# Kernel tuning notes

Hardware: AMD Instinct MI355X
Metric: run time of the kernel (lower is better)

## Reference

```python
import jax, jax.numpy as jnp
import numpy as np

N_HEAD = 16
EPS = 1e-6


def setup_inputs() -> dict:
    key = jax.random.key(0)
    k1, k2, k3 = jax.random.split(key, 3)
    B, T, C = 2, 2048, 1024
    x = jax.random.normal(k1, (B, T, C), dtype=jnp.float32)
    w_attn = jax.random.normal(k2, (C, 3 * C), dtype=jnp.float32) * 0.02
    w_proj = jax.random.normal(k3, (C, C), dtype=jnp.float32) * 0.02
    return {"x": x, "w_attn": w_attn, "w_proj": w_proj}


def _linear_attention(q, k, v):
    """q,k,v: (T,B,H,D) with q,k already feature-mapped (elu+1).
    Causal linear attention via a D x D running-state recurrence (same math
    as cumsum of k-v outer products, computed without the O(T*D^2) tensor)."""
    B, H, D = q.shape[1], q.shape[2], q.shape[3]

    def step(carry, qkv_t):
        S, z = carry                      # S:(B,H,D,D), z:(B,H,D)
        qt, kt, vt = qkv_t                # each (B,H,D)
        S = S + kt[..., :, None] * vt[..., None, :]
        z = z + kt
        num = jnp.einsum('bhi,bhij->bhj', qt, S)
        den = jnp.sum(qt * z, axis=-1, keepdims=True)
        return (S, z), num / (den + EPS)

    S0 = jnp.zeros((B, H, D, D), q.dtype)
    z0 = jnp.zeros((B, H, D), q.dtype)
    _, y = jax.lax.scan(step, (S0, z0), (q, k, v))
    return y                              # (T,B,H,D)


def reference(x, w_attn, w_proj):
    B, T, C = x.shape
    H = N_HEAD
    D = C // H
    qkv = x @ w_attn                      # (B,T,3C)
    q, k, v = jnp.split(qkv, 3, axis=-1)

    def to_tbhd(a):                       # (B,T,C) -> (T,B,H,D)
        return a.reshape(B, T, H, D).transpose(1, 0, 2, 3)

    q = jax.nn.elu(to_tbhd(q)) + 1.0      # phi(x) = ELU(x)+1
    k = jax.nn.elu(to_tbhd(k)) + 1.0
    v = to_tbhd(v)

    y = _linear_attention(q, k, v)        # (T,B,H,D)
    y = y.transpose(1, 0, 2, 3).reshape(B, T, C)
    return y @ w_proj                     # resid dropout p=0.0 is identity
```

## Files before the change

kernel.cpp:

```cpp
#include <hip/hip_runtime.h>
#include <hip/hip_bf16.h>
#include <cmath>

#define TB   2048
#define CCH  1024
#define NCH  32
#define EPSF 1e-6f

typedef unsigned short u16;
typedef __attribute__((ext_vector_type(8))) short  frag8;
typedef __attribute__((ext_vector_type(4))) float  floatx4;

__device__ __forceinline__ u16 f2bf(float f) {
    unsigned int u = __float_as_uint(f);
    unsigned int r = (u + 0x7fffu + ((u >> 16) & 1u)) >> 16;
    return (u16)r;
}
__device__ __forceinline__ float bf2f(u16 v) {
    return __uint_as_float(((unsigned int)v) << 16);
}

__device__ __forceinline__ void async_load16(const u16* g, u16* l) {
    __builtin_amdgcn_global_load_lds(
        (const __attribute__((address_space(1))) void*)g,
        (__attribute__((address_space(3))) void*)l,
        16, 0, 0);
}

__global__ __launch_bounds__(256) void prep_k(
    const float* __restrict__ x, const float* __restrict__ wa,
    const float* __restrict__ wp,
    u16* __restrict__ xb, u16* __restrict__ waT, u16* __restrict__ wpT)
{
    __shared__ u16 t[64][72];
    int blk = blockIdx.x;
    if (blk < 2048) {
        int i = (blk * 256 + threadIdx.x) * 8;
        float4 a = *(const float4*)(x + i);
        float4 b = *(const float4*)(x + i + 4);
        u16 v[8];
        v[0] = f2bf(a.x); v[1] = f2bf(a.y); v[2] = f2bf(a.z); v[3] = f2bf(a.w);
        v[4] = f2bf(b.x); v[5] = f2bf(b.y); v[6] = f2bf(b.z); v[7] = f2bf(b.w);
        *(uint4*)(xb + i) = *(uint4*)v;
        return;
    }
    const float* in; u16* out; int K, N, bx, by;
    if (blk < 2048 + 768) {
        int tb = blk - 2048; in = wa; out = waT; K = 1024; N = 3072;
        bx = tb % 48; by = tb / 48;
    } else {
        int tb = blk - 2816; in = wp; out = wpT; K = 1024; N = 1024;
        bx = tb & 15; by = tb >> 4;
    }
    const int k0 = by * 64, n0 = bx * 64;
    #pragma unroll
    for (int i = 0; i < 4; ++i) {
        int rr = (threadIdx.x >> 4) + 16 * i;
        int c4 = (threadIdx.x & 15) * 4;
        float4 v = *(const float4*)(in + (size_t)(k0 + rr) * N + n0 + c4);
        t[c4 + 0][rr] = f2bf(v.x);
        t[c4 + 1][rr] = f2bf(v.y);
        t[c4 + 2][rr] = f2bf(v.z);
        t[c4 + 3][rr] = f2bf(v.w);
    }
    __syncthreads();
    #pragma unroll
    for (int i = 0; i < 2; ++i) {
        int rr = (threadIdx.x >> 3) + 32 * i;
        int c8 = (threadIdx.x & 7) * 8;
        u16 o[8];
        #pragma unroll
        for (int q = 0; q < 8; ++q) o[q] = t[rr][c8 + q];
        *(uint4*)(out + (size_t)(n0 + rr) * K + k0 + c8) = *(uint4*)o;
    }
}

__global__ __launch_bounds__(256) void gemm_bf16_bf16out_k(
    const u16* __restrict__ A, const u16* __restrict__ BT,
    u16* __restrict__ C, int N, int K, int phi_cols)
{
    __shared__ u16 Als[128 * 64];
    __shared__ u16 Bls[128 * 64];
    const int tid  = threadIdx.x;
    const int wave = tid >> 6, lane = tid & 63;
    const int quad = lane >> 4, lrow = lane & 15;
    const int wm = wave >> 1, wn = wave & 1;
    const int row0 = blockIdx.y * 128, col0 = blockIdx.x * 128;
    const int lr = lane >> 3;
    const int lc = ((lane & 7) ^ lr) * 8;
    const int rsw = lrow & 7;
    floatx4 acc[4][4] = {};

    for (int k0 = 0; k0 < K; k0 += 64) {
        __syncthreads();
        #pragma unroll
        for (int m = 0; m < 4; ++m) {
            int i = wave * 4 + m;
            async_load16(A  + (size_t)(row0 + i * 8 + lr) * K + k0 + lc, &Als[i * 512]);
            async_load16(BT + (size_t)(col0 + i * 8 + lr) * K + k0 + lc, &Bls[i * 512]);
        }
        __syncthreads();
        #pragma unroll
        for (int ksi = 0; ksi < 2; ++ksi) {
            frag8 af[4], bf[4];
            #pragma unroll
            for (int i = 0; i < 4; ++i)
                af[i] = *(const frag8*)&Als[(wm * 64 + i * 16 + lrow) * 64
                                            + ((ksi * 4 + quad) ^ rsw) * 8];
            #pragma unroll
            for (int i = 0; i < 4; ++i)
                bf[i] = *(const frag8*)&Bls[(wn * 64 + i * 16 + lrow) * 64
                                            + ((ksi * 4 + quad) ^ rsw) * 8];
            #pragma unroll
            for (int i = 0; i < 4; ++i)
                #pragma unroll
                for (int jn = 0; jn < 4; ++jn)
                    acc[i][jn] = __builtin_amdgcn_mfma_f32_16x16x32_bf16(
                        af[i], bf[jn], acc[i][jn], 0, 0, 0);
        }
    }

    #pragma unroll
    for (int i = 0; i < 4; ++i) {
        #pragma unroll
        for (int jn = 0; jn < 4; ++jn) {
            int col = col0 + wn * 64 + jn * 16 + lrow;
            bool isphi = col < phi_cols;
            #pragma unroll
            for (int r = 0; r < 4; ++r) {
                int row = row0 + wm * 64 + i * 16 + quad * 4 + r;
                float v = acc[i][jn][r];
                if (isphi) v = (v > 0.f) ? (v + 1.f) : __expf(v);
                C[(size_t)row * N + col] = f2bf(v);
            }
        }
    }
}

__global__ __launch_bounds__(256) void gemm_bf16_f32out_k(
    const u16* __restrict__ A, const u16* __restrict__ BT,
    float* __restrict__ C, int N, int K)
{
    __shared__ u16 Als[128 * 128];
    __shared__ u16 Bls[64 * 128];
    const int tid  = threadIdx.x;
    const int wave = tid >> 6, lane = tid & 63;
    const int quad = lane >> 4, lrow = lane & 15;
    const int wm = wave >> 1, wn = wave & 1;
    const int row0 = blockIdx.y * 128, col0 = blockIdx.x * 64;
    const int lr4 = lane >> 4;
    floatx4 acc[4][2] = {};

    for (int k0 = 0; k0 < K; k0 += 128) {
        __syncthreads();
        #pragma unroll
        for (int m = 0; m < 8; ++m) {
            int rbase = wave * 32 + m * 4;
            int cg = (lane & 15) ^ ((rbase + lr4) & 15);
            async_load16(A + (size_t)(row0 + rbase + lr4) * K + k0 + cg * 8,
                         &Als[rbase * 128]);
        }
        #pragma unroll
        for (int m = 0; m < 4; ++m) {
            int rbase = wave * 16 + m * 4;
            int cg = (lane & 15) ^ ((rbase + lr4) & 15);
            async_load16(BT + (size_t)(col0 + rbase + lr4) * K + k0 + cg * 8,
                         &Bls[rbase * 128]);
        }
        __syncthreads();
        #pragma unroll
        for (int ksi = 0; ksi < 4; ++ksi) {
            frag8 af[4], bf[2];
            #pragma unroll
            for (int i = 0; i < 4; ++i)
                af[i] = *(const frag8*)&Als[(wm * 64 + i * 16 + lrow) * 128
                                            + ((ksi * 4 + quad) ^ lrow) * 8];
            #pragma unroll
            for (int jn = 0; jn < 2; ++jn)
                bf[jn] = *(const frag8*)&Bls[(wn * 32 + jn * 16 + lrow) * 128
                                             + ((ksi * 4 + quad) ^ lrow) * 8];
            #pragma unroll
            for (int i = 0; i < 4; ++i)
                #pragma unroll
                for (int jn = 0; jn < 2; ++jn)
                    acc[i][jn] = __builtin_amdgcn_mfma_f32_16x16x32_bf16(
                        af[i], bf[jn], acc[i][jn], 0, 0, 0);
        }
    }

    #pragma unroll
    for (int i = 0; i < 4; ++i)
        #pragma unroll
        for (int jn = 0; jn < 2; ++jn) {
            int col = col0 + wn * 32 + jn * 16 + lrow;
            #pragma unroll
            for (int r = 0; r < 4; ++r) {
                int row = row0 + wm * 64 + i * 16 + quad * 4 + r;
                C[(size_t)row * N + col] = acc[i][jn][r];
            }
        }
}

__global__ __launch_bounds__(256) void chunk_kv_mfma_k(
    const u16* __restrict__ qkv,
    u16* __restrict__ Spt,
    float* __restrict__ zloc,
    u16* __restrict__ VtG)
{
    __shared__ u16 Kt[64][72];
    __shared__ u16 Vt[64][72];
    const int tid  = threadIdx.x;
    const int wave = tid >> 6, lane = tid & 63;
    const int quad = lane >> 4, lrow = lane & 15;
    const int blk = blockIdx.x;
    const int c = blk & 31, h = (blk >> 5) & 15, b = blk >> 9;
    const int t0 = c * 64;
    const u16* base = qkv + (size_t)(b * TB + t0) * 3072 + h * 64;

    #pragma unroll
    for (int m = 0; m < 2; ++m) {
        int chunk = tid + 256 * m;
        int s = chunk >> 3, d0 = (chunk & 7) * 8;
        const u16* row = base + (size_t)s * 3072;
        u16 kv[8], vv[8];
        *(uint4*)kv = *(const uint4*)(row + 1024 + d0);
        *(uint4*)vv = *(const uint4*)(row + 2048 + d0);
        #pragma unroll
        for (int q = 0; q < 8; ++q) { Kt[d0 + q][s] = kv[q]; Vt[d0 + q][s] = vv[q]; }
    }
    __syncthreads();

    #pragma unroll
    for (int m = 0; m < 2; ++m) {
        int e = tid + 256 * m;
        int r = e >> 3, c8 = (e & 7) * 8;
        u16 o[8];
        #pragma unroll
        for (int q = 0; q < 8; ++q) o[q] = Vt[r][c8 + q];
        *(uint4*)(VtG + (size_t)blk * 4096 + r * 64 + c8) = *(uint4*)o;
    }

    frag8 vf[2];
    #pragma unroll
    for (int ks = 0; ks < 2; ++ks)
        vf[ks] = *(const frag8*)&Vt[wave * 16 + lrow][ks * 32 + quad * 8];
    u16* So = Spt + (size_t)blk * 4096;
    #pragma unroll
    for (int jn = 0; jn < 4; ++jn) {
        floatx4 acc = {};
        #pragma unroll
        for (int ks = 0; ks < 2; ++ks) {
            frag8 kf = *(const frag8*)&Kt[jn * 16 + lrow][ks * 32 + quad * 8];
            acc = __builtin_amdgcn_mfma_f32_16x16x32_bf16(vf[ks], kf, acc, 0, 0, 0);
        }
        #pragma unroll
        for (int r = 0; r < 4; ++r) {
            int j = wave * 16 + quad * 4 + r;
            int i = jn * 16 + lrow;
            So[j * 64 + i] = f2bf(acc[r]);
        }
    }
    if (tid < 64) {
        float z = 0.f;
        for (int s = 0; s < 64; ++s) z += bf2f(Kt[tid][s]);
        zloc[(size_t)blk * 64 + tid] = z;
    }
}

__global__ __launch_bounds__(256) void scan_state_k(
    u16* __restrict__ Spt, float* __restrict__ z)
{
    const int bh = blockIdx.x >> 1;
    const int part = blockIdx.x & 1;
    const int e0 = part * 2048 + threadIdx.x * 8;
    const size_t base = (size_t)bh * NCH * 4096;
    float r[8] = {};
    for (int c = 0; c < NCH; ++c) {
        u16* p = Spt + base + (size_t)c * 4096 + e0;
        u16 t[8];
        *(uint4*)t = *(const uint4*)p;
        u16 o[8];
        #pragma unroll
        for (int q = 0; q < 8; ++q) { o[q] = f2bf(r[q]); r[q] += bf2f(t[q]); }
        *(uint4*)p = *(uint4*)o;
    }
    if (part == 0 && threadIdx.x < 64) {
        const size_t zb = (size_t)bh * NCH * 64;
        float rz = 0.f;
        for (int c = 0; c < NCH; ++c) {
            float t = z[zb + c * 64 + threadIdx.x];
            z[zb + c * 64 + threadIdx.x] = rz;
            rz += t;
        }
    }
}

__global__ __launch_bounds__(256) void attn_mfma_k(
    const u16* __restrict__ qkv,
    const u16* __restrict__ SptG,
    const float* __restrict__ zp,
    const u16* __restrict__ VtG,
    u16* __restrict__ Yb)
{
    __shared__ u16 Qls[64 * 64];
    __shared__ u16 Kls[64 * 64];
    __shared__ u16 Vls[64 * 64];
    __shared__ u16 Sls[64 * 64];
    __shared__ float zps[64];
    __shared__ float den4[64][4];
    __shared__ float den[64];

    const int tid  = threadIdx.x;
    const int wave = tid >> 6, lane = tid & 63;
    const int quad = lane >> 4, lrow = lane & 15;
    const int blk = blockIdx.x;
    const int c = blk & 31, h = (blk >> 5) & 15, b = blk >> 9;
    const int t0 = c * 64;
    const int lr = lane >> 3;
    const int lc = ((lane & 7) ^ lr) * 8;
    const int rsw = lrow & 7;
    const u16* qbase = qkv + (size_t)(b * TB + t0) * 3072 + h * 64;

    #pragma unroll
    for (int m = 0; m < 2; ++m) {
        int i = wave * 2 + m;
        int r = i * 8 + lr;
        async_load16(qbase + (size_t)r * 3072 + lc,          &Qls[i * 512]);
        async_load16(qbase + (size_t)r * 3072 + 1024 + lc,   &Kls[i * 512]);
        async_load16(SptG + (size_t)blk * 4096 + r * 64 + lc, &Sls[i * 512]);
        async_load16(VtG  + (size_t)blk * 4096 + r * 64 + lc, &Vls[i * 512]);
    }
    if (tid < 64) zps[tid] = zp[(size_t)blk * 64 + tid];
    __syncthreads();

    frag8 qf[2];
    #pragma unroll
    for (int ks = 0; ks < 2; ++ks)
        qf[ks] = *(const frag8*)&Qls[(wave * 16 + lrow) * 64 + ((ks * 4 + quad) ^ rsw) * 8];

    floatx4 yacc[4] = {}, kacc[4] = {};
    #pragma unroll
    for (int jn = 0; jn < 4; ++jn) {
        #pragma unroll
        for (int ks = 0; ks < 2; ++ks) {
            frag8 spf = *(const frag8*)&Sls[(jn * 16 + lrow) * 64 + ((ks * 4 + quad) ^ rsw) * 8];
            yacc[jn] = __builtin_amdgcn_mfma_f32_16x16x32_bf16(qf[ks], spf, yacc[jn], 0, 0, 0);
            frag8 kf = *(const frag8*)&Kls[(jn * 16 + lrow) * 64 + ((ks * 4 + quad) ^ rsw) * 8];
            kacc[jn] = __builtin_amdgcn_mfma_f32_16x16x32_bf16(qf[ks], kf, kacc[jn], 0, 0, 0);
        }
    }
    __syncthreads();

    #pragma unroll
    for (int jn = 0; jn < 4; ++jn) {
        int s = jn * 16 + lrow;
        #pragma unroll
        for (int r = 0; r < 4; ++r) {
            int t = wave * 16 + quad * 4 + r;
            float v = (s <= t) ? kacc[jn][r] : 0.f;
            Sls[t * 64 + (((s >> 3) ^ (t & 7)) * 8) + (s & 7)] = f2bf(v);
        }
    }
    __syncthreads();

    {
        int t = tid >> 2, seg = tid & 3;
        float p = 0.f;
        #pragma unroll
        for (int g2 = 0; g2 < 2; ++g2) {
            int g = seg * 2 + g2;
            int pq = ((g ^ (t & 7)) * 8);
            const u16* qp = &Qls[t * 64 + pq];
            const u16* ap = &Sls[t * 64 + pq];
            #pragma unroll
            for (int e = 0; e < 8; ++e) {
                p += bf2f(qp[e]) * zps[g * 8 + e] + bf2f(ap[e]);
            }
        }
        den4[t][seg] = p;
    }

    frag8 af2[2];
    #pragma unroll
    for (int ks = 0; ks < 2; ++ks)
        af2[ks] = *(const frag8*)&Sls[(wave * 16 + lrow) * 64 + ((ks * 4 + quad) ^ rsw) * 8];
    #pragma unroll
    for (int jn = 0; jn < 4; ++jn)
        #pragma unroll
        for (int ks = 0; ks < 2; ++ks) {
            frag8 vf = *(const frag8*)&Vls[(jn * 16 + lrow) * 64 + ((ks * 4 + quad) ^ rsw) * 8];
            yacc[jn] = __builtin_amdgcn_mfma_f32_16x16x32_bf16(af2[ks], vf, yacc[jn], 0, 0, 0);
        }
    __syncthreads();
    if (tid < 64) den[tid] = den4[tid][0] + den4[tid][1] + den4[tid][2] + den4[tid][3];
    __syncthreads();

    #pragma unroll
    for (int jn = 0; jn < 4; ++jn) {
        #pragma unroll
        for (int r = 0; r < 4; ++r) {
            int t = wave * 16 + quad * 4 + r;
            float inv = 1.f / (den[t] + EPSF);
            Qls[t * 64 + jn * 16 + lrow] = f2bf(yacc[jn][r] * inv);
        }
    }
    __syncthreads();
    {
        int row = tid >> 2, seg = tid & 3;
        size_t o = (size_t)(b * TB + t0 + row) * CCH + h * 64 + seg * 16;
        *(uint4*)(Yb + o)     = *(uint4*)&Qls[row * 64 + seg * 16];
        *(uint4*)(Yb + o + 8) = *(uint4*)&Qls[row * 64 + seg * 16 + 8];
    }
}

extern "C" void kernel_launch(void* const* d_in, const int* in_sizes, int n_in,
                              void* d_out, int out_size, void* d_ws, size_t ws_size,
                              hipStream_t stream)
{
    const float* x      = (const float*)d_in[0];
    const float* w_attn = (const float*)d_in[1];
    const float* w_proj = (const float*)d_in[2];
    float* out = (float*)d_out;

    u16* xb    = (u16*)d_ws;
    u16* waT   = xb    + (size_t)4096 * 1024;
    u16* wpT   = waT   + (size_t)3072 * 1024;
    u16* Yb    = wpT   + (size_t)1024 * 1024;
    u16* qkv_b = Yb    + (size_t)4096 * 1024;
    u16* Spt   = qkv_b + (size_t)4096 * 3072;
    u16* VtG   = Spt   + (size_t)1024 * 4096;
    float* zloc = (float*)(VtG + (size_t)1024 * 4096);

    prep_k<<<3072, 256, 0, stream>>>(x, w_attn, w_proj, xb, waT, wpT);

    gemm_bf16_bf16out_k<<<dim3(24, 32), 256, 0, stream>>>(xb, waT, qkv_b, 3072, 1024, 2048);

    chunk_kv_mfma_k<<<1024, 256, 0, stream>>>(qkv_b, Spt, zloc, VtG);
    scan_state_k   <<<64,   256, 0, stream>>>(Spt, zloc);
    attn_mfma_k    <<<1024, 256, 0, stream>>>(qkv_b, Spt, zloc, VtG, Yb);

    gemm_bf16_f32out_k<<<dim3(16, 32), 256, 0, stream>>>(Yb, wpT, out, 1024, 1024);
}
```

Baseline: 169.6 us.

## Double-buffer LDS tiles in bf16 GEMM to overlap global loads with MFMA

Converts the QKV/projection GEMM main loop to double-buffered shared memory. The next K-tile is fetched with async global-to-LDS loads while the current tile is consumed, using explicit vmcnt waits and barriers. This is meant to hide global load latency behind MFMA work. It doubles LDS use to 64KB per block, which may reduce occupancy, and it relies on hand-counted waitcnt values being correct.

```diff
diff --git a/kernel.cpp b/kernel.cpp
--- a/kernel.cpp
+++ b/kernel.cpp
@@ -79,8 +79,8 @@
     const u16* __restrict__ A, const u16* __restrict__ BT,
     u16* __restrict__ C, int N, int K, int phi_cols)
 {
-    __shared__ u16 Als[128 * 64];
-    __shared__ u16 Bls[128 * 64];
+    __shared__ u16 Als[2][128 * 64];
+    __shared__ u16 Bls[2][128 * 64];
     const int tid  = threadIdx.x;
     const int wave = tid >> 6, lane = tid & 63;
     const int quad = lane >> 4, lrow = lane & 15;
@@ -90,27 +90,46 @@
     const int lc = ((lane & 7) ^ lr) * 8;
     const int rsw = lrow & 7;
     floatx4 acc[4][4] = {};
-
-    for (int k0 = 0; k0 < K; k0 += 64) {
-        __syncthreads();
-        #pragma unroll
-        for (int m = 0; m < 4; ++m) {
-            int i = wave * 4 + m;
-            async_load16(A  + (size_t)(row0 + i * 8 + lr) * K + k0 + lc, &Als[i * 512]);
-            async_load16(BT + (size_t)(col0 + i * 8 + lr) * K + k0 + lc, &Bls[i * 512]);
-        }
-        __syncthreads();
+    const int NT = K >> 6;
+
+    #pragma unroll
+    for (int m = 0; m < 4; ++m) {
+        int i = wave * 4 + m;
+        async_load16(A  + (size_t)(row0 + i * 8 + lr) * K + lc, &Als[0][i * 512]);
+        async_load16(BT + (size_t)(col0 + i * 8 + lr) * K + lc, &Bls[0][i * 512]);
+    }
+
+    for (int t = 0; t < NT; ++t) {
+        const int p = t & 1;
+        if (t + 1 < NT) {
+            const int k0 = (t + 1) << 6;
+            #pragma unroll
+            for (int m = 0; m < 4; ++m) {
+                int i = wave * 4 + m;
+                async_load16(A  + (size_t)(row0 + i * 8 + lr) * K + k0 + lc,
+                             &Als[p ^ 1][i * 512]);
+                async_load16(BT + (size_t)(col0 + i * 8 + lr) * K + k0 + lc,
+                             &Bls[p ^ 1][i * 512]);
+            }
+            __builtin_amdgcn_sched_barrier(0);
+            asm volatile("s_waitcnt vmcnt(8)" ::: "memory");
+        } else {
+            asm volatile("s_waitcnt vmcnt(0)" ::: "memory");
+        }
+        __builtin_amdgcn_s_barrier();
+        __builtin_amdgcn_sched_barrier(0);
+
         #pragma unroll
         for (int ksi = 0; ksi < 2; ++ksi) {
             frag8 af[4], bf[4];
             #pragma unroll
             for (int i = 0; i < 4; ++i)
-                af[i] = *(const frag8*)&Als[(wm * 64 + i * 16 + lrow) * 64
-                                            + ((ksi * 4 + quad) ^ rsw) * 8];
+                af[i] = *(const frag8*)&Als[p][(wm * 64 + i * 16 + lrow) * 64
+                                              + ((ksi * 4 + quad) ^ rsw) * 8];
             #pragma unroll
             for (int i = 0; i < 4; ++i)
-                bf[i] = *(const frag8*)&Bls[(wn * 64 + i * 16 + lrow) * 64
-                                            + ((ksi * 4 + quad) ^ rsw) * 8];
+                bf[i] = *(const frag8*)&Bls[p][(wn * 64 + i * 16 + lrow) * 64
+                                              + ((ksi * 4 + quad) ^ rsw) * 8];
             #pragma unroll
             for (int i = 0; i < 4; ++i)
                 #pragma unroll
@@ -118,6 +137,10 @@
                     acc[i][jn] = __builtin_amdgcn_mfma_f32_16x16x32_bf16(
                         af[i], bf[jn], acc[i][jn], 0, 0, 0);
         }
+
+        asm volatile("s_waitcnt lgkmcnt(0)" ::: "memory");
+        __builtin_amdgcn_sched_barrier(0);
+        __builtin_amdgcn_s_barrier();
     }
 
     #pragma unroll
```

After: 166.8 us. Within noise of the previous version (-1.7%).

## Rewrite QKV GEMM as 256x256 tile, 8-wave, double-buffered pipelined kernel

Applied to the files above, without the earlier changes.

Replaces the 128x128 QKV projection GEMM with a 256x256-tile kernel using 512 threads, double-buffered LDS, and an 8-phase schedule. Each phase interleaves async global-to-LDS loads of the next k-tile halves with MFMA work, using explicit vmcnt waits, sched barriers and setprio. Block IDs are swizzled for L2 locality. The aim is to hide load latency and raise arithmetic intensity, at the cost of more LDS and registers per block (launch bounds 512,2) and only 192 blocks, which is fewer than the CU count.

```diff
diff --git a/kernel.cpp b/kernel.cpp
--- a/kernel.cpp
+++ b/kernel.cpp
@@ -75,63 +75,117 @@
     }
 }
 
-__global__ __launch_bounds__(256) void gemm_bf16_bf16out_k(
-    const u16* __restrict__ A, const u16* __restrict__ BT,
-    u16* __restrict__ C, int N, int K, int phi_cols)
-{
-    __shared__ u16 Als[128 * 64];
-    __shared__ u16 Bls[128 * 64];
+#define PHASE(P, STAGE_STMT, VMW) do {                                        \
+    frag8 af[4][2], bf[2][2];                                                 \
+    _Pragma("unroll")                                                         \
+    for (int m = 0; m < 4; ++m)                                               \
+      _Pragma("unroll")                                                       \
+      for (int kk = 0; kk < 2; ++kk)                                          \
+        af[m][kk] = *(const frag8*)&Abuf[(P) >= 4][(((P) >> 1) & 1) * 8192    \
+            + (wm * 64 + m * 16 + lrow) * 64 + (((kk * 4 + quad) ^ rsw) * 8)];\
+    _Pragma("unroll")                                                         \
+    for (int n = 0; n < 2; ++n)                                               \
+      _Pragma("unroll")                                                       \
+      for (int kk = 0; kk < 2; ++kk)                                          \
+        bf[n][kk] = *(const frag8*)&Bbuf[(P) >= 4][((P) & 1) * 8192           \
+            + (wn * 32 + n * 16 + lrow) * 64 + (((kk * 4 + quad) ^ rsw) * 8)];\
+    STAGE_STMT;                                                               \
+    __builtin_amdgcn_sched_barrier(0);                                        \
+    if (VMW) asm volatile("s_waitcnt vmcnt(4)" ::: "memory");                 \
+    __builtin_amdgcn_s_barrier();                                             \
+    __builtin_amdgcn_sched_barrier(0);                                        \
+    __builtin_amdgcn_s_setprio(1);                                            \
+    _Pragma("unroll")                                                         \
+    for (int m = 0; m < 4; ++m)                                               \
+      _Pragma("unroll")                                                       \
+      for (int n = 0; n < 2; ++n)                                             \
+        _Pragma("unroll")                                                     \
+        for (int kk = 0; kk < 2; ++kk)                                        \
+          acc[(((P) >> 1) & 1) * 4 + m][((P) & 1) * 2 + n] =                  \
+            __builtin_amdgcn_mfma_f32_16x16x32_bf16(                          \
+              af[m][kk], bf[n][kk],                                           \
+              acc[(((P) >> 1) & 1) * 4 + m][((P) & 1) * 2 + n], 0, 0, 0);     \
+    __builtin_amdgcn_s_setprio(0);                                            \
+    __builtin_amdgcn_sched_barrier(0);                                        \
+    __builtin_amdgcn_s_barrier();                                             \
+  } while (0)
+
+__global__ __launch_bounds__(512, 2) void gemm1_256_k(
+    const u16* __restrict__ Ag, const u16* __restrict__ BTg,
+    u16* __restrict__ Cg, int N, int K, int phi_cols)
+{
+    __shared__ u16 Abuf[2][16384];
+    __shared__ u16 Bbuf[2][16384];
     const int tid  = threadIdx.x;
     const int wave = tid >> 6, lane = tid & 63;
     const int quad = lane >> 4, lrow = lane & 15;
-    const int wm = wave >> 1, wn = wave & 1;
-    const int row0 = blockIdx.y * 128, col0 = blockIdx.x * 128;
+    const int wm = wave >> 2, wn = wave & 3;
     const int lr = lane >> 3;
     const int lc = ((lane & 7) ^ lr) * 8;
     const int rsw = lrow & 7;
-    floatx4 acc[4][4] = {};
-
-    for (int k0 = 0; k0 < K; k0 += 64) {
-        __syncthreads();
-        #pragma unroll
-        for (int m = 0; m < 4; ++m) {
-            int i = wave * 4 + m;
-            async_load16(A  + (size_t)(row0 + i * 8 + lr) * K + k0 + lc, &Als[i * 512]);
-            async_load16(BT + (size_t)(col0 + i * 8 + lr) * K + k0 + lc, &Bls[i * 512]);
-        }
-        __syncthreads();
-        #pragma unroll
-        for (int ksi = 0; ksi < 2; ++ksi) {
-            frag8 af[4], bf[4];
-            #pragma unroll
-            for (int i = 0; i < 4; ++i)
-                af[i] = *(const frag8*)&Als[(wm * 64 + i * 16 + lrow) * 64
-                                            + ((ksi * 4 + quad) ^ rsw) * 8];
-            #pragma unroll
-            for (int i = 0; i < 4; ++i)
-                bf[i] = *(const frag8*)&Bls[(wn * 64 + i * 16 + lrow) * 64
-                                            + ((ksi * 4 + quad) ^ rsw) * 8];
-            #pragma unroll
-            for (int i = 0; i < 4; ++i)
-                #pragma unroll
-                for (int jn = 0; jn < 4; ++jn)
-                    acc[i][jn] = __builtin_amdgcn_mfma_f32_16x16x32_bf16(
-                        af[i], bf[jn], acc[i][jn], 0, 0, 0);
-        }
-    }
-
-    #pragma unroll
-    for (int i = 0; i < 4; ++i) {
-        #pragma unroll
-        for (int jn = 0; jn < 4; ++jn) {
-            int col = col0 + wn * 64 + jn * 16 + lrow;
+    const int NKT = K >> 6;
+
+    int bid = blockIdx.x;
+    int swz = (bid & 7) * 24 + (bid >> 3);
+    int by = swz / 12, bx = swz - by * 12;
+    const int row0 = by * 256, col0 = bx * 256;
+
+    floatx4 acc[8][4] = {};
+
+    auto stageA = [&](int kt, int hh) {
+        int ktc = kt < NKT ? kt : NKT - 1;
+        u16* dst = &Abuf[ktc & 1][hh * 8192];
+        #pragma unroll
+        for (int m2 = 0; m2 < 2; ++m2) {
+            int i = wave * 2 + m2;
+            int lrid = i * 8 + lr;
+            int grow = row0 + (lrid & 63) + hh * 64 + ((lrid >> 6) << 7);
+            async_load16(Ag + (size_t)grow * K + ktc * 64 + lc, dst + i * 512);
+        }
+    };
+    auto stageB = [&](int kt, int hh) {
+        int ktc = kt < NKT ? kt : NKT - 1;
+        u16* dst = &Bbuf[ktc & 1][hh * 8192];
+        #pragma unroll
+        for (int m2 = 0; m2 < 2; ++m2) {
+            int i = wave * 2 + m2;
+            int lrid = i * 8 + lr;
+            int gcol = col0 + (lrid & 31) + hh * 32 + ((lrid >> 5) << 6);
+            async_load16(BTg + (size_t)gcol * K + ktc * 64 + lc, dst + i * 512);
+        }
+    };
+
+    stageA(0, 0); stageB(0, 0); stageA(0, 1); stageB(0, 1);
+    stageA(1, 0); stageB(1, 0);
+    __builtin_amdgcn_sched_barrier(0);
+    asm volatile("s_waitcnt vmcnt(4)" ::: "memory");
+    __builtin_amdgcn_s_barrier();
+    __builtin_amdgcn_sched_barrier(0);
+
+    for (int it = 0; it < (NKT >> 1); ++it) {
+        const int ka = it * 2, kb = ka + 1;
+        PHASE(0, stageA(kb, 1),     false);
+        PHASE(1, stageB(kb, 1),     false);
+        PHASE(2, stageA(ka + 2, 0), false);
+        PHASE(3, stageB(ka + 2, 0), true);
+        PHASE(4, stageA(ka + 2, 1), false);
+        PHASE(5, stageB(ka + 2, 1), false);
+        PHASE(6, stageA(kb + 2, 0), false);
+        PHASE(7, stageB(kb + 2, 0), true);
+    }
+
+    #pragma unroll
+    for (int M = 0; M < 8; ++M) {
+        #pragma unroll
+        for (int NN = 0; NN < 4; ++NN) {
+            int col = col0 + wn * 64 + (NN >> 1) * 32 + (NN & 1) * 16 + lrow;
             bool isphi = col < phi_cols;
             #pragma unroll
             for (int r = 0; r < 4; ++r) {
-                int row = row0 + wm * 64 + i * 16 + quad * 4 + r;
-                float v = acc[i][jn][r];
+                int row = row0 + wm * 128 + (M >> 2) * 64 + (M & 3) * 16 + quad * 4 + r;
+                float v = acc[M][NN][r];
                 if (isphi) v = (v > 0.f) ? (v + 1.f) : __expf(v);
-                C[(size_t)row * N + col] = f2bf(v);
+                Cg[(size_t)row * N + col] = f2bf(v);
             }
         }
     }
@@ -433,7 +487,7 @@
 
     prep_k<<<3072, 256, 0, stream>>>(x, w_attn, w_proj, xb, waT, wpT);
 
-    gemm_bf16_bf16out_k<<<dim3(24, 32), 256, 0, stream>>>(xb, waT, qkv_b, 3072, 1024, 2048);
+    gemm1_256_k<<<192, 512, 0, stream>>>(xb, waT, qkv_b, 3072, 1024, 2048);
 
     chunk_kv_mfma_k<<<1024, 256, 0, stream>>>(qkv_b, Spt, zloc, VtG);
     scan_state_k   <<<64,   256, 0, stream>>>(Spt, zloc);
```

Measured after the change: 169.9 us. No clear change (+0.2%).
